# Optimization experiments

Hardware: AMD Instinct MI355X
Metric: run time of the kernel (lower is better)

Reference implementation:

```python
import jax, jax.numpy as jnp
import numpy as np

NUM_HEADS = 8
BLOCK = 16


def setup_inputs() -> dict:
    key = jax.random.key(0)
    kx, k1, k2, k3 = jax.random.split(key, 4)
    B, S, D = 8, 8192, 512
    x = jax.random.normal(kx, (B, S, D), dtype=jnp.float32)
    # nn.MultiheadAttention parameters (xavier-ish scale)
    w_in = jax.random.normal(k1, (3 * D, D), dtype=jnp.float32) / np.sqrt(D)
    b_in = jnp.zeros((3 * D,), dtype=jnp.float32)
    w_out = jax.random.normal(k2, (D, D), dtype=jnp.float32) / np.sqrt(D)
    b_out = jnp.zeros((D,), dtype=jnp.float32)
    return {"x": x, "w_in": w_in, "b_in": b_in, "w_out": w_out, "b_out": b_out}


def reference(x, w_in, b_in, w_out, b_out):
    B, S, D = x.shape
    H = NUM_HEADS
    hd = D // H
    nb = S // BLOCK
    # [B, nb, L, D] — independent attention within each length-BLOCK chunk
    xb = x.reshape(B, nb, BLOCK, D)
    qkv = jnp.einsum('bnld,ed->bnle', xb, w_in) + b_in  # e = 3D
    q, k, v = jnp.split(qkv, 3, axis=-1)
    q = q.reshape(B, nb, BLOCK, H, hd)
    k = k.reshape(B, nb, BLOCK, H, hd)
    v = v.reshape(B, nb, BLOCK, H, hd)
    scale = 1.0 / np.sqrt(hd).astype(np.float32)
    scores = jnp.einsum('bnqhd,bnkhd->bnhqk', q * scale, k)
    attn = jax.nn.softmax(scores, axis=-1)
    ctx = jnp.einsum('bnhqk,bnkhd->bnqhd', attn, v).reshape(B, nb, BLOCK, D)
    out = jnp.einsum('bnld,od->bnlo', ctx, w_out) + b_out
    return out.reshape(B, S, D)
```

## Files before the change

### kernel.cpp

```cpp
#include <hip/hip_runtime.h>
#include <hip/hip_bf16.h>

typedef __attribute__((ext_vector_type(4))) float f32x4;
typedef __attribute__((ext_vector_type(8))) short short8;
typedef __attribute__((ext_vector_type(4))) short short4v;
using bf16 = __hip_bfloat16;

__device__ __forceinline__ short f2bf(float x) {
  union { bf16 h; short s; } u;
  u.h = __float2bfloat16(x);
  return u.s;
}

__device__ __forceinline__ void gload16(const void* g, void* l) {
  __builtin_amdgcn_global_load_lds(
      (const __attribute__((address_space(1))) void*)g,
      (__attribute__((address_space(3))) void*)l, 16, 0, 0);
}

__global__ void cvt_f32_to_bf16(const float* __restrict__ src,
                                bf16* __restrict__ dst, int n4) {
  int i = blockIdx.x * blockDim.x + threadIdx.x;
  const int stride = gridDim.x * blockDim.x;
  for (; i < n4; i += stride) {
    f32x4 v = ((const f32x4*)src)[i];
    short4v o;
    o[0] = f2bf(v[0]); o[1] = f2bf(v[1]); o[2] = f2bf(v[2]); o[3] = f2bf(v[3]);
    ((short4v*)dst)[i] = o;
  }
}

template<bool OUT_BF16>
__global__ __launch_bounds__(512) void gemm_bt(
    const bf16* __restrict__ A, int lda,
    const bf16* __restrict__ B, int ldb,
    const float* __restrict__ bias,
    void* __restrict__ Cv, int ldc, int nbx)
{
  __shared__ __align__(16) bf16 lA[4][256 * 32];
  __shared__ __align__(16) bf16 lB[4][256 * 32];

  const int tid  = threadIdx.x;
  const int lane = tid & 63;
  const int w    = tid >> 6;
  const int wr   = w >> 2;
  const int wc   = w & 3;
  const int l15  = lane & 15;
  const int kg   = lane >> 4;
  const int po   = (kg ^ ((l15 >> 1) & 3)) * 8;

  const int nwg = gridDim.x;
  const int dd  = blockIdx.x;
  const int wid = (dd & 7) * (nwg >> 3) + (dd >> 3);
  const size_t bm = (size_t)(wid / nbx) * 256;
  const size_t bn = (size_t)(wid % nbx) * 256;

  const int srow = w * 16 + (lane >> 2);
  const int scol = ((lane & 3) ^ ((lane >> 3) & 3)) * 8;
  const int wofs = w * 512;

  const bf16* Ab = A + (bm + srow) * lda + scol;
  const bf16* Bb = B + (bn + srow) * ldb + scol;

  f32x4 acc[8][4];
#pragma unroll
  for (int i = 0; i < 8; ++i)
#pragma unroll
    for (int j = 0; j < 4; ++j) acc[i][j] = (f32x4)0.f;

  short8 af[8], bq[4];

#define SA(buf, h, kt) gload16(Ab + (size_t)((h) * 128) * lda + (kt), \
                               &lA[buf][(h) * 4096 + wofs])
#define SB(buf, h, kt) gload16(Bb + (size_t)((h) * 128) * ldb + (kt), \
                               &lB[buf][(h) * 4096 + wofs])

#define CLOSE_V(N) do { \
    __builtin_amdgcn_sched_barrier(0); \
    asm volatile("s_waitcnt vmcnt(" #N ")" ::: "memory"); \
    __builtin_amdgcn_sched_barrier(0); \
    __builtin_amdgcn_s_barrier(); \
    __builtin_amdgcn_sched_barrier(0); \
    asm volatile("" ::: "memory"); } while (0)

  SA(0, 0, 0);  SA(0, 1, 0);  SB(0, 0, 0);  SB(0, 1, 0);
  SA(1, 0, 32); SA(1, 1, 32); SB(1, 0, 32); SB(1, 1, 32);
  SA(2, 0, 64); SA(2, 1, 64); SB(2, 0, 64); SB(2, 1, 64);
  CLOSE_V(8);

#pragma unroll
  for (int t = 0; t < 16; ++t) {
    const int cur = t & 3, pf = (t + 3) & 3;
    const int kt3 = (t + 3) * 32;

#pragma unroll
    for (int mi = 0; mi < 8; ++mi)
      af[mi] = *(const short8*)&lA[cur][(wr * 128 + mi * 16 + l15) * 32 + po];
#pragma unroll
    for (int ni = 0; ni < 4; ++ni)
      bq[ni] = *(const short8*)&lB[cur][(wc * 64 + ni * 16 + l15) * 32 + po];

    if (t < 13) { SA(pf, 0, kt3); SB(pf, 0, kt3); }

    __builtin_amdgcn_s_setprio(1);
#pragma unroll
    for (int mi = 0; mi < 4; ++mi)
#pragma unroll
      for (int ni = 0; ni < 4; ++ni)
        acc[mi][ni] = __builtin_amdgcn_mfma_f32_16x16x32_bf16(
            bq[ni], af[mi], acc[mi][ni], 0, 0, 0);
    __builtin_amdgcn_s_setprio(0);

    if (t < 13) { SA(pf, 1, kt3); SB(pf, 1, kt3); }

    __builtin_amdgcn_s_setprio(1);
#pragma unroll
    for (int mi = 4; mi < 8; ++mi)
#pragma unroll
      for (int ni = 0; ni < 4; ++ni)
        acc[mi][ni] = __builtin_amdgcn_mfma_f32_16x16x32_bf16(
            bq[ni], af[mi], acc[mi][ni], 0, 0, 0);
    __builtin_amdgcn_s_setprio(0);

    if (t <= 12)      CLOSE_V(8);
    else if (t == 13) CLOSE_V(4);
    else if (t == 14) CLOSE_V(0);
  }

#undef SA
#undef SB
#undef CLOSE_V

#pragma unroll
  for (int mi = 0; mi < 8; ++mi) {
    const size_t mrow = bm + wr * 128 + mi * 16 + l15;
#pragma unroll
    for (int ni = 0; ni < 4; ++ni) {
      const int nb = (int)bn + wc * 64 + ni * 16 + kg * 4;
      f32x4 bv = *(const f32x4*)&bias[nb];
      f32x4 r = acc[mi][ni] + bv;
      if constexpr (OUT_BF16) {
        short4v o;
        o[0] = f2bf(r[0]); o[1] = f2bf(r[1]); o[2] = f2bf(r[2]); o[3] = f2bf(r[3]);
        *(short4v*)((bf16*)Cv + mrow * ldc + nb) = o;
      } else {
        *(f32x4*)((float*)Cv + mrow * ldc + nb) = r;
      }
    }
  }
}

__global__ __launch_bounds__(256) void attn_kernel(bf16* __restrict__ qkv)
{
  const int tid  = threadIdx.x;
  const int wave = tid >> 6;
  const int lane = tid & 63;
  const int l15  = lane & 15;
  const int kg   = lane >> 4;
  const size_t mbase = (size_t)blockIdx.x * 16;

  f32x4 ctxv[2][4];

#pragma unroll
  for (int hi = 0; hi < 2; ++hi) {
    const int h = wave + hi * 4;
    const bf16* qp = qkv + (mbase + l15) * 1536 + h * 64 + kg * 8;
    short8 qf0 = *(const short8*)qp;
    short8 qf1 = *(const short8*)(qp + 32);
    short8 kf0 = *(const short8*)(qp + 512);
    short8 kf1 = *(const short8*)(qp + 544);

    f32x4 st = (f32x4)0.f;
    st = __builtin_amdgcn_mfma_f32_16x16x32_bf16(kf0, qf0, st, 0, 0, 0);
    st = __builtin_amdgcn_mfma_f32_16x16x32_bf16(kf1, qf1, st, 0, 0, 0);

    float s[4];
#pragma unroll
    for (int r = 0; r < 4; ++r) s[r] = st[r] * 0.125f;
    float mx = fmaxf(fmaxf(s[0], s[1]), fmaxf(s[2], s[3]));
    mx = fmaxf(mx, __shfl_xor(mx, 16));
    mx = fmaxf(mx, __shfl_xor(mx, 32));
    float p[4], sum = 0.f;
#pragma unroll
    for (int r = 0; r < 4; ++r) { p[r] = __expf(s[r] - mx); sum += p[r]; }
    sum += __shfl_xor(sum, 16);
    sum += __shfl_xor(sum, 32);
    const float inv = 1.f / sum;

    short4v pf;
#pragma unroll
    for (int r = 0; r < 4; ++r) pf[r] = f2bf(p[r] * inv);

    const bf16* vp = qkv + mbase * 1536 + 1024 + h * 64;
#pragma unroll
    for (int dt = 0; dt < 4; ++dt) {
      short4v vf;
#pragma unroll
      for (int jj = 0; jj < 4; ++jj)
        vf[jj] = *(const short*)(vp + (size_t)(kg * 4 + jj) * 1536 + dt * 16 + l15);
      f32x4 c = (f32x4)0.f;
      c = __builtin_amdgcn_mfma_f32_16x16x16bf16_1k(pf, vf, c, 0, 0, 0);
      ctxv[hi][dt] = c;
    }
  }

  __syncthreads();

#pragma unroll
  for (int hi = 0; hi < 2; ++hi) {
    const int h = wave + hi * 4;
#pragma unroll
    for (int dt = 0; dt < 4; ++dt) {
#pragma unroll
      for (int r = 0; r < 4; ++r) {
        ((short*)qkv)[(mbase + kg * 4 + r) * 1536 + h * 64 + dt * 16 + l15] =
            f2bf(ctxv[hi][dt][r]);
      }
    }
  }
}

extern "C" void kernel_launch(void* const* d_in, const int* in_sizes, int n_in,
                              void* d_out, int out_size, void* d_ws, size_t ws_size,
                              hipStream_t stream) {
  (void)in_sizes; (void)n_in; (void)out_size; (void)ws_size;
  const float* x     = (const float*)d_in[0];
  const float* w_in  = (const float*)d_in[1];
  const float* b_in  = (const float*)d_in[2];
  const float* w_out = (const float*)d_in[3];
  const float* b_out = (const float*)d_in[4];
  float* out = (float*)d_out;

  char* ws = (char*)d_ws;
  bf16* qkv   = (bf16*)ws;
  bf16* winb  = (bf16*)(ws + (size_t)65536 * 1536 * 2);
  bf16* woutb = (bf16*)(ws + (size_t)65536 * 1536 * 2 + (size_t)786432 * 2);
  bf16* xb = (bf16*)d_out;

  cvt_f32_to_bf16<<<768, 256, 0, stream>>>(w_in, winb, 786432 / 4);
  cvt_f32_to_bf16<<<256, 256, 0, stream>>>(w_out, woutb, 262144 / 4);
  cvt_f32_to_bf16<<<4096, 256, 0, stream>>>(x, xb, (65536 * 512) / 4);

  gemm_bt<true><<<1536, 512, 0, stream>>>(
      xb, 512, winb, 512, b_in, (void*)qkv, 1536, 6);

  attn_kernel<<<4096, 256, 0, stream>>>(qkv);

  gemm_bt<false><<<512, 512, 0, stream>>>(
      qkv, 1536, woutb, 512, b_out, (void*)out, 512, 2);
}
```

Measured before the change: 288.3 us.

## Fuse block attention with output projection through LDS-staged context

Merges the attention kernel and the output-projection GEMM into one kernel. Each 512-thread workgroup computes the bf16 context for 64 rows into a swizzled LDS tile, then multiplies it directly by w_out and adds the bias. This removes the global round-trip of the context tensor and one launch. In exchange, w_out fragments are read straight from global/L2 with no LDS staging or pipelining, and the workgroup needs 64 KB of LDS, which limits occupancy.

```diff
diff --git a/kernel.cpp b/kernel.cpp
--- a/kernel.cpp
+++ b/kernel.cpp
@@ -150,21 +150,25 @@
   }
 }
 
-__global__ __launch_bounds__(256) void attn_kernel(bf16* __restrict__ qkv)
+__global__ __launch_bounds__(512) void attn_out_kernel(
+    const bf16* __restrict__ qkv, const bf16* __restrict__ woutb,
+    const float* __restrict__ b_out, float* __restrict__ out)
 {
+  __shared__ __align__(16) bf16 ctx_lds[64][512];
+
   const int tid  = threadIdx.x;
-  const int wave = tid >> 6;
+  const int w    = tid >> 6;
   const int lane = tid & 63;
   const int l15  = lane & 15;
   const int kg   = lane >> 4;
-  const size_t mbase = (size_t)blockIdx.x * 16;
-
-  f32x4 ctxv[2][4];
-
-#pragma unroll
-  for (int hi = 0; hi < 2; ++hi) {
-    const int h = wave + hi * 4;
-    const bf16* qp = qkv + (mbase + l15) * 1536 + h * 64 + kg * 8;
+  const size_t mbase = (size_t)blockIdx.x * 64;
+  const int blk = w >> 1;
+  const size_t rbase = mbase + blk * 16;
+
+#pragma unroll
+  for (int hi = 0; hi < 4; ++hi) {
+    const int h = (w & 1) * 4 + hi;
+    const bf16* qp = qkv + (rbase + l15) * 1536 + h * 64 + kg * 8;
     short8 qf0 = *(const short8*)qp;
     short8 qf1 = *(const short8*)(qp + 32);
     short8 kf0 = *(const short8*)(qp + 512);
@@ -191,7 +195,7 @@
 #pragma unroll
     for (int r = 0; r < 4; ++r) pf[r] = f2bf(p[r] * inv);
 
-    const bf16* vp = qkv + mbase * 1536 + 1024 + h * 64;
+    const bf16* vp = qkv + rbase * 1536 + 1024 + h * 64;
 #pragma unroll
     for (int dt = 0; dt < 4; ++dt) {
       short4v vf;
@@ -199,23 +203,53 @@
       for (int jj = 0; jj < 4; ++jj)
         vf[jj] = *(const short*)(vp + (size_t)(kg * 4 + jj) * 1536 + dt * 16 + l15);
       f32x4 c = (f32x4)0.f;
-      c = __builtin_amdgcn_mfma_f32_16x16x16bf16_1k(pf, vf, c, 0, 0, 0);
-      ctxv[hi][dt] = c;
+      c = __builtin_amdgcn_mfma_f32_16x16x16bf16_1k(vf, pf, c, 0, 0, 0);
+      short4v o;
+#pragma unroll
+      for (int r = 0; r < 4; ++r) o[r] = f2bf(c[r]);
+      const int slot = h * 8 + dt * 2 + (kg >> 1);
+      const int col  = ((slot ^ (l15 & 7)) << 3) | ((kg & 1) * 4);
+      *(short4v*)&ctx_lds[blk * 16 + l15][col] = o;
     }
   }
 
   __syncthreads();
 
-#pragma unroll
-  for (int hi = 0; hi < 2; ++hi) {
-    const int h = wave + hi * 4;
-#pragma unroll
-    for (int dt = 0; dt < 4; ++dt) {
-#pragma unroll
-      for (int r = 0; r < 4; ++r) {
-        ((short*)qkv)[(mbase + kg * 4 + r) * 1536 + h * 64 + dt * 16 + l15] =
-            f2bf(ctxv[hi][dt][r]);
-      }
+  f32x4 acc[4][4];
+#pragma unroll
+  for (int i = 0; i < 4; ++i)
+#pragma unroll
+    for (int j = 0; j < 4; ++j) acc[i][j] = (f32x4)0.f;
+
+#pragma unroll
+  for (int kc = 0; kc < 16; ++kc) {
+    short8 wf[4], cf[4];
+#pragma unroll
+    for (int ni = 0; ni < 4; ++ni)
+      wf[ni] = *(const short8*)&woutb[(size_t)(w * 64 + ni * 16 + l15) * 512 +
+                                      kc * 32 + kg * 8];
+#pragma unroll
+    for (int mi = 0; mi < 4; ++mi) {
+      const int row  = mi * 16 + l15;
+      const int slot = kc * 4 + kg;
+      cf[mi] = *(const short8*)&ctx_lds[row][((slot ^ (l15 & 7)) << 3)];
+    }
+#pragma unroll
+    for (int mi = 0; mi < 4; ++mi)
+#pragma unroll
+      for (int ni = 0; ni < 4; ++ni)
+        acc[mi][ni] = __builtin_amdgcn_mfma_f32_16x16x32_bf16(
+            wf[ni], cf[mi], acc[mi][ni], 0, 0, 0);
+  }
+
+#pragma unroll
+  for (int mi = 0; mi < 4; ++mi) {
+    const size_t mrow = mbase + mi * 16 + l15;
+#pragma unroll
+    for (int ni = 0; ni < 4; ++ni) {
+      const int nb = w * 64 + ni * 16 + kg * 4;
+      f32x4 bv = *(const f32x4*)&b_out[nb];
+      *(f32x4*)&out[mrow * 512 + nb] = acc[mi][ni] + bv;
     }
   }
 }
@@ -244,8 +278,5 @@
   gemm_bt<true><<<1536, 512, 0, stream>>>(
       xb, 512, winb, 512, b_in, (void*)qkv, 1536, 6);
 
-  attn_kernel<<<4096, 256, 0, stream>>>(qkv);
-
-  gemm_bt<false><<<512, 512, 0, stream>>>(
-      qkv, 1536, woutb, 512, b_out, (void*)out, 512, 2);
-}
+  attn_out_kernel<<<1024, 512, 0, stream>>>(qkv, woutb, b_out, out);
+}
```

New measurement: 294.7 us. +2.2%, slower.
